# Kernel tuning notes

Hardware: AMD Instinct MI355X
Metric: run time of the kernel (lower is better)

Reference implementation:

```python
import jax, jax.numpy as jnp
import numpy as np

TEMP = 0.1          # temp1 == base_temperature -> scale factor temp/base = 1
N_VIEW = 100        # max_views


def _select_indices(hard, easy):
    """Deterministic analogue of _hard_anchor_sampling's per-(image,class) pick.
    hard, easy: [M, HW] bool. Returns [M, N_VIEW] pixel indices (hard first,
    then easy, in pixel-index order; torch uses randperm but the contrastive
    loss is invariant to which/ordering of in-set samples)."""
    half = N_VIEW // 2
    nh = hard.sum(-1)
    ne = easy.sum(-1)
    both = (nh >= half) & (ne >= half)
    hk = jnp.where(both, half, jnp.where(nh >= half, N_VIEW - ne, nh))  # num_hard_keep
    ek = N_VIEW - hk                                                     # num_easy_keep
    hrank = jnp.cumsum(hard.astype(jnp.int32), -1) - 1
    erank = jnp.cumsum(easy.astype(jnp.int32), -1) - 1
    sel = (hard & (hrank < hk[:, None])) | (easy & (erank < ek[:, None]))
    # stable argsort puts selected pixels first, preserving index order
    order = jnp.argsort(jnp.where(sel, 0, 1), axis=-1)
    return order[:, :N_VIEW]


def _contrastive(feats_, labels_):
    """feats_: [A, V, D], labels_: [A] float. Supervised contrastive loss."""
    A, V, D = feats_.shape
    N = A * V
    # torch.cat(torch.unbind(feats_, 1), 0) -> view-major ordering
    cf = feats_.transpose(1, 0, 2).reshape(N, D)
    lab = jnp.tile(labels_, V)                           # mask.repeat(V, V)
    mask = (lab[:, None] == lab[None, :]).astype(cf.dtype)
    logits = (cf @ cf.T) / TEMP                          # [N, N]
    logits = logits - jax.lax.stop_gradient(logits.max(axis=1, keepdims=True))
    neg_mask = 1.0 - mask                                # before removing diagonal
    pos_mask = mask * (1.0 - jnp.eye(N, dtype=cf.dtype)) # logits_mask zeroes diag
    exp_l = jnp.exp(logits)
    neg_sum = (exp_l * neg_mask).sum(axis=1, keepdims=True)
    log_prob = logits - jnp.log(exp_l + neg_sum)
    mean_log_prob_pos = (pos_mask * log_prob).sum(axis=1) / pos_mask.sum(axis=1)
    return -(TEMP / TEMP) * mean_log_prob_pos.mean()


def _forward(feats, predict, labels):
    B, D, H, W = feats.shape
    C = predict.shape[1]
    HW = H * W
    # F.normalize(feats, p=2, dim=1)
    norm = jnp.sqrt((feats * feats).sum(axis=1, keepdims=True))
    feats = feats / jnp.maximum(norm, 1e-12)
    # bilinear upsample of logits to (H, W), softmax, conf/argmax
    logits_up = jax.image.resize(predict, (B, C, H, W), method='linear')
    probs = jax.nn.softmax(logits_up, axis=1)
    pred = jnp.argmax(probs, axis=1)                     # [B, H, W] (conf unused by loss)
    # nearest resize of labels to (H, W) is identity here (same size)
    pred_f = pred.reshape(B, HW)
    lab_f = labels.reshape(B, HW)
    feats_f = feats.transpose(0, 2, 3, 1).reshape(B, HW, D)
    cls = jnp.arange(C)
    hard = (pred_f[:, None, :] == cls[None, :, None]) & (lab_f[:, None, :] != cls[None, :, None])
    easy = (pred_f[:, None, :] == cls[None, :, None]) & (lab_f[:, None, :] == cls[None, :, None])
    idx = _select_indices(hard.reshape(B * C, HW), easy.reshape(B * C, HW))  # [B*C, N_VIEW]
    b_idx = jnp.repeat(jnp.arange(B), C)
    X_ = feats_f[b_idx[:, None], idx]                    # [B*C, N_VIEW, D]
    y_ = jnp.tile(cls, B).astype(feats.dtype)            # [B*C]
    return _contrastive(X_, y_)


def setup_inputs() -> dict:
    key = jax.random.key(0)
    k1, k2, k3 = jax.random.split(key, 3)
    feats = jax.random.normal(k1, (4, 256, 128, 128), dtype=jnp.float32)
    predict = jax.random.normal(k2, (4, 21, 64, 64), dtype=jnp.float32)
    labels = jax.random.randint(k3, (4, 128, 128), 0, 21, dtype=jnp.int32)
    return {"feats": feats, "predict": predict, "labels": labels}


def reference(feats, predict, labels):
    return _forward(feats, predict, labels)
```

## Files before the change

kernel.cpp:

```cpp
#include <hip/hip_runtime.h>
#include <math.h>

#define HW 16384
#define WID 128
#define BB 4
#define CC 21
#define DD 256
#define NA 84
#define NV 100
#define NN 8400
#define NPOS 400
#define NPAD 8448
#define NTILE 66
#define NTRI 2211
#define NPOSBLK (16 * CC)

typedef __bf16 bf16;
typedef bf16 v8bf __attribute__((ext_vector_type(8)));
typedef float v4f __attribute__((ext_vector_type(4)));

#define AS1(p) ((const __attribute__((address_space(1))) void*)(p))
#define AS3(p) ((__attribute__((address_space(3))) void*)(p))

__global__ void pred_kernel(const float* __restrict__ predict, int* __restrict__ pred) {
  int t = blockIdx.x * blockDim.x + threadIdx.x;
  int b = t / HW;
  int p = t % HW;
  int y = p / WID, x = p % WID;
  float yin = y * 0.5f - 0.25f;
  float xin = x * 0.5f - 0.25f;
  int y0 = (int)floorf(yin), x0 = (int)floorf(xin);
  float fy = yin - (float)y0, fx = xin - (float)x0;
  int y0c = max(y0, 0), y1c = min(y0 + 1, 63);
  int x0c = max(x0, 0), x1c = min(x0 + 1, 63);
  float w00 = (1.f - fy) * (1.f - fx), w01 = (1.f - fy) * fx;
  float w10 = fy * (1.f - fx),        w11 = fy * fx;
  const float* pb = predict + (size_t)b * CC * 4096;
  float best = -1e30f; int bc = 0;
  for (int c = 0; c < CC; ++c) {
    const float* pc = pb + c * 4096;
    float v = w00 * pc[y0c * 64 + x0c] + w01 * pc[y0c * 64 + x1c]
            + w10 * pc[y1c * 64 + x0c] + w11 * pc[y1c * 64 + x1c];
    if (v > best) { best = v; bc = c; }
  }
  pred[t] = bc;
}

__global__ __launch_bounds__(256) void select_kernel(const int* __restrict__ pred,
                                                     const int* __restrict__ labels,
                                                     int* __restrict__ idx) {
  int pair = blockIdx.x;
  int b = pair / CC, c = pair % CC;
  int tid = threadIdx.x;
  const int4* pb = (const int4*)(pred + b * HW) + tid * 16;
  const int4* lb = (const int4*)(labels + b * HW) + tid * 16;

  unsigned long long hm = 0ull, em = 0ull;
  #pragma unroll
  for (int g = 0; g < 16; ++g) {
    int4 p4 = pb[g];
    int4 l4 = lb[g];
    unsigned long long h =
        ((unsigned long long)((p4.x == c) & (l4.x != c)))      |
        ((unsigned long long)((p4.y == c) & (l4.y != c)) << 1) |
        ((unsigned long long)((p4.z == c) & (l4.z != c)) << 2) |
        ((unsigned long long)((p4.w == c) & (l4.w != c)) << 3);
    unsigned long long e =
        ((unsigned long long)((p4.x == c) & (l4.x == c)))      |
        ((unsigned long long)((p4.y == c) & (l4.y == c)) << 1) |
        ((unsigned long long)((p4.z == c) & (l4.z == c)) << 2) |
        ((unsigned long long)((p4.w == c) & (l4.w == c)) << 3);
    hm |= h << (g * 4);
    em |= e << (g * 4);
  }
  int nh_t = __popcll(hm), ne_t = __popcll(em);

  __shared__ int sh[256], se[256], ss[256];
  sh[tid] = nh_t; se[tid] = ne_t;
  __syncthreads();
  for (int off = 1; off < 256; off <<= 1) {
    int vh = (tid >= off) ? sh[tid - off] : 0;
    int ve = (tid >= off) ? se[tid - off] : 0;
    __syncthreads();
    sh[tid] += vh; se[tid] += ve;
    __syncthreads();
  }
  int h_excl = sh[tid] - nh_t, e_excl = se[tid] - ne_t;
  int nh = sh[255], ne = se[255];

  const int half = NV / 2;
  int hk;
  if (nh >= half && ne >= half) hk = half;
  else if (nh >= half)          hk = NV - ne;
  else                          hk = nh;
  int ek = NV - hk;

  int takeh = min(max(hk - h_excl, 0), nh_t);
  int takee = min(max(ek - e_excl, 0), ne_t);
  int sel_t = takeh + takee;
  ss[tid] = sel_t;
  __syncthreads();
  for (int off = 1; off < 256; off <<= 1) {
    int vs = (tid >= off) ? ss[tid - off] : 0;
    __syncthreads();
    ss[tid] += vs;
    __syncthreads();
  }
  int s_excl = ss[tid] - sel_t;
  int total_sel = ss[255];
  int F = NV - total_sel;
  int u_excl = tid * 64 - s_excl;

  int* out = idx + pair * NV;
  int sc = 0, uc = 0, hc = 0, ec = 0;
  for (int l = 0; l < 64; ++l) {
    int p = tid * 64 + l;
    int hard = (int)((hm >> l) & 1ull);
    int easy = (int)((em >> l) & 1ull);
    bool sel = (hard && hc < takeh) || (easy && ec < takee);
    hc += hard; ec += easy;
    if (sel) {
      if (s_excl + sc < NV) out[s_excl + sc] = p;
      sc++;
    } else {
      if (u_excl + uc < F) out[total_sel + u_excl + uc] = p;
      uc++;
    }
  }
}

__global__ __launch_bounds__(256) void gather_kernel(const float* __restrict__ feats,
                                                     const int* __restrict__ idx,
                                                     bf16* __restrict__ cf) {
  int g = blockIdx.x;
  int d = threadIdx.x;
  if (g == 2100) {
    v8bf z = {};
    for (int e = d; e < (NPAD - NN) * DD / 8; e += 256)
      *(v8bf*)(cf + (size_t)NN * DD + e * 8) = z;
    return;
  }
  int a = g % NA;
  int v0 = (g / NA) * 4;
  int b = a / CC;

  int p[4];
  #pragma unroll
  for (int k = 0; k < 4; ++k) p[k] = idx[a * NV + v0 + k];
  const float* base = feats + (size_t)(b * DD + d) * HW;
  float val[4], ssk[4];
  #pragma unroll
  for (int k = 0; k < 4; ++k) { val[k] = base[p[k]]; ssk[k] = val[k] * val[k]; }

  #pragma unroll
  for (int k = 0; k < 4; ++k) {
    float s = ssk[k];
    s += __shfl_xor(s, 1);  s += __shfl_xor(s, 2);  s += __shfl_xor(s, 4);
    s += __shfl_xor(s, 8);  s += __shfl_xor(s, 16); s += __shfl_xor(s, 32);
    ssk[k] = s;
  }
  __shared__ float red[4][4];
  if ((d & 63) == 0) {
    #pragma unroll
    for (int k = 0; k < 4; ++k) red[d >> 6][k] = ssk[k];
  }
  __syncthreads();
  #pragma unroll
  for (int k = 0; k < 4; ++k) {
    float tot = red[0][k] + red[1][k] + red[2][k] + red[3][k];
    float inv = 1.0f / fmaxf(sqrtf(tot), 1e-12f);
    int n = (v0 + k) * NA + a;
    cf[(size_t)n * DD + d] = (bf16)(val[k] * inv);
  }
}

__global__ __launch_bounds__(256) void gemm_kernel(const bf16* __restrict__ cf,
                                                   float* __restrict__ row_part,
                                                   float* __restrict__ s_pos) {
  __shared__ __align__(16) bf16 smem[2 * 128 * 64];
  bf16* sA = smem;
  bf16* sB = smem + 128 * 64;
  int blk = blockIdx.x;
  bool pos = blk >= NTRI;
  int i0, j0, c = 0, I = 0, J = 0;
  bool diag = false;
  if (!pos) {
    I = (int)((sqrtf(8.0f * blk + 1.0f) - 1.0f) * 0.5f);
    while ((I + 1) * (I + 2) / 2 <= blk) ++I;
    while (I * (I + 1) / 2 > blk) --I;
    J = blk - I * (I + 1) / 2;
    i0 = I * 128;
    j0 = J * 128;
    diag = (I == J);
  } else {
    int pb = blk - NTRI;
    c = pb / 16;
    int bx = pb % 16;
    i0 = (bx >> 2) * 128;
    j0 = (bx & 3) * 128;
  }
  int tid = threadIdx.x;
  int wave = tid >> 6, lane = tid & 63;
  int wi = wave >> 1, wj = wave & 1;
  int m = lane & 15, q = lane >> 4;

  v4f acc[4][4] = {};

  int lrow = lane >> 3;
  int cxor = (lane & 7) ^ lrow;

  for (int k0 = 0; k0 < DD; k0 += 64) {
    #pragma unroll
    for (int it = 0; it < 4; ++it) {
      int row = wave * 32 + it * 8;
      int ri = i0 + row + lrow, rj = j0 + row + lrow;
      int gi, gj;
      if (!pos) { gi = ri; gj = rj; }
      else {
        gi = (ri < NPOS) ? ((ri >> 2) * NA + (ri & 3) * CC + c) : NN;
        gj = (rj < NPOS) ? ((rj >> 2) * NA + (rj & 3) * CC + c) : NN;
      }
      __builtin_amdgcn_global_load_lds(AS1(cf + (size_t)gi * DD + k0 + cxor * 8),
                                       AS3(sA + row * 64), 16, 0, 0);
      __builtin_amdgcn_global_load_lds(AS1(cf + (size_t)gj * DD + k0 + cxor * 8),
                                       AS3(sB + row * 64), 16, 0, 0);
    }
    __syncthreads();
    #pragma unroll
    for (int kk = 0; kk < 2; ++kk) {
      v8bf af[4], bfr[4];
      #pragma unroll
      for (int tt = 0; tt < 4; ++tt) {
        int r = wi * 64 + tt * 16 + m;
        af[tt] = *(const v8bf*)(sA + r * 64 + (((kk * 4 + q) ^ (m & 7)) * 8));
      }
      #pragma unroll
      for (int tt = 0; tt < 4; ++tt) {
        int r = wj * 64 + tt * 16 + m;
        bfr[tt] = *(const v8bf*)(sB + r * 64 + (((kk * 4 + q) ^ (m & 7)) * 8));
      }
      #pragma unroll
      for (int ti = 0; ti < 4; ++ti)
        #pragma unroll
        for (int tj = 0; tj < 4; ++tj)
          acc[ti][tj] = __builtin_amdgcn_mfma_f32_16x16x32_bf16(af[ti], bfr[tj], acc[ti][tj], 0, 0, 0);
    }
    __syncthreads();
  }

  if (!pos) {
    int iw0 = i0 + wi * 64;
    int jw0 = j0 + wj * 64;
    float rowp[16];
    float colp[4] = {0.f, 0.f, 0.f, 0.f};
    #pragma unroll
    for (int tt = 0; tt < 16; ++tt) rowp[tt] = 0.f;

    #pragma unroll
    for (int ti = 0; ti < 4; ++ti) {
      #pragma unroll
      for (int r = 0; r < 4; ++r) {
        int i = iw0 + ti * 16 + q * 4 + r;
        bool iok = (i < NN);
        #pragma unroll
        for (int tj = 0; tj < 4; ++tj) {
          int j = jw0 + tj * 16 + m;
          float e = __expf(acc[ti][tj][r] * 10.0f - 10.0f);
          if (j < NN) rowp[ti * 4 + r] += e;
          if (!diag && iok) colp[tj] += e;
        }
      }
    }

    float* redR = (float*)smem;
    float* redC = (float*)smem + 128 * 33;
    #pragma unroll
    for (int ti = 0; ti < 4; ++ti)
      #pragma unroll
      for (int r = 0; r < 4; ++r) {
        int rg = wi * 64 + ti * 16 + q * 4 + r;
        redR[rg * 33 + wj * 16 + m] = rowp[ti * 4 + r];
      }
    if (!diag) {
      #pragma unroll
      for (int tj = 0; tj < 4; ++tj) {
        int cg = wj * 64 + tj * 16 + m;
        redC[cg * 9 + wi * 4 + q] = colp[tj];
      }
    }
    __syncthreads();
    if (tid < 128) {
      float s = 0.f;
      #pragma unroll
      for (int t = 0; t < 32; ++t) s += redR[tid * 33 + t];
      row_part[(size_t)J * NPAD + i0 + tid] = s;
      if (!diag) {
        float s2 = 0.f;
        #pragma unroll
        for (int t = 0; t < 8; ++t) s2 += redC[tid * 9 + t];
        row_part[(size_t)I * NPAD + j0 + tid] = s2;
      }
    }
  } else {
    #pragma unroll
    for (int ti = 0; ti < 4; ++ti) {
      #pragma unroll
      for (int r = 0; r < 4; ++r) {
        int ri = i0 + wi * 64 + ti * 16 + q * 4 + r;
        if (ri >= NPOS) continue;
        int gi = (ri >> 2) * NA + (ri & 3) * CC + c;
        #pragma unroll
        for (int tj = 0; tj < 4; ++tj) {
          int rj = j0 + wj * 64 + tj * 16 + m;
          if (rj < NPOS)
            s_pos[(size_t)gi * NPOS + rj] = acc[ti][tj][r] * 10.0f - 10.0f;
        }
      }
    }
  }
}

__global__ __launch_bounds__(256) void loss_kernel(const float* __restrict__ s_pos,
                                                   const float* __restrict__ row_part,
                                                   double* __restrict__ partials) {
  int tid = threadIdx.x;
  int wave = tid >> 6, lane = tid & 63;
  int i = blockIdx.x * 4 + wave;
  const float* row = s_pos + (size_t)i * NPOS;

  float nsum = 0.f;
  for (int jb = lane; jb < NTILE; jb += 64)
    nsum += row_part[(size_t)jb * NPAD + i];

  float sp[7], ev[7];
  float psum = 0.f;
  #pragma unroll
  for (int t = 0; t < 7; ++t) {
    int k = lane + t * 64;
    if (k < NPOS) {
      sp[t] = row[k];
      ev[t] = __expf(sp[t]);
      psum += ev[t];
    } else { sp[t] = 0.f; ev[t] = 0.f; }
  }
  float comb = nsum - psum;
  for (int o = 32; o; o >>= 1) comb += __shfl_xor(comb, o);
  float ns = comb;

  int self = (i / NA) * 4 + ((i % NA) / CC);
  float tsum = 0.f;
  #pragma unroll
  for (int t = 0; t < 7; ++t) {
    int k = lane + t * 64;
    if (k < NPOS && k != self)
      tsum += sp[t] - __logf(ev[t] + ns);
  }
  for (int o = 32; o; o >>= 1) tsum += __shfl_xor(tsum, o);

  __shared__ float r2[4];
  if (lane == 0) r2[wave] = tsum;
  __syncthreads();
  if (tid == 0) partials[blockIdx.x] = (double)(r2[0] + r2[1] + r2[2] + r2[3]);
}

__global__ void final_kernel(const double* __restrict__ partials, float* __restrict__ out) {
  int lane = threadIdx.x;
  double s = 0.0;
  for (int t = lane; t < 2100; t += 64) s += partials[t];
  for (int o = 32; o; o >>= 1) s += __shfl_down(s, o);
  if (lane == 0) out[0] = (float)(-s / 399.0 / 8400.0);
}

extern "C" void kernel_launch(void* const* d_in, const int* in_sizes, int n_in,
                              void* d_out, int out_size, void* d_ws, size_t ws_size,
                              hipStream_t stream) {
  const float* feats   = (const float*)d_in[0];
  const float* predict = (const float*)d_in[1];
  const int*   labels  = (const int*)d_in[2];
  float* out = (float*)d_out;
  char* ws = (char*)d_ws;

  int*    pred     = (int*)(ws + 0);
  int*    idx      = (int*)(ws + 262144);
  float*  row_part = (float*)(ws + 295744);
  double* partials = (double*)(ws + 2526016);
  bf16*   cf       = (bf16*)(ws + 2542816);
  float*  s_pos    = (float*)(ws + 6868192);

  pred_kernel<<<256, 256, 0, stream>>>(predict, pred);
  select_kernel<<<NA, 256, 0, stream>>>(pred, labels, idx);
  gather_kernel<<<2101, 256, 0, stream>>>(feats, idx, cf);
  gemm_kernel<<<NTRI + NPOSBLK, 256, 0, stream>>>(cf, row_part, s_pos);
  loss_kernel<<<2100, 256, 0, stream>>>(s_pos, row_part, partials);
  final_kernel<<<1, 64, 0, stream>>>(partials, out);
}
```

Baseline: 185.4 us.

## Stream feats in coalesced pixel chunks via inverse index map instead of scattered gather

The index list is replaced by an inverse map from pixel to output row. The gather kernel now streams all of feats in coalesced 32-pixel chunks through shared memory, normalizes each pixel and writes only the mapped pixels. Unselected filler samples go through an atomic-appended fill list handled by dedicated blocks. This swaps strided scalar reads for full, coalesced reads of the feature tensor, and adds extra bandwidth plus an atomic counter.

```diff
diff --git a/kernel.cpp b/kernel.cpp
--- a/kernel.cpp
+++ b/kernel.cpp
@@ -14,16 +14,23 @@
 #define NTILE 66
 #define NTRI 2211
 #define NPOSBLK (16 * CC)
+#define PXC 32
+#define NCHUNK (BB * HW / PXC)
+#define NFILLB 84
 
 typedef __bf16 bf16;
 typedef bf16 v8bf __attribute__((ext_vector_type(8)));
+typedef bf16 v4bf __attribute__((ext_vector_type(4)));
 typedef float v4f __attribute__((ext_vector_type(4)));
 
 #define AS1(p) ((const __attribute__((address_space(1))) void*)(p))
 #define AS3(p) ((__attribute__((address_space(3))) void*)(p))
 
-__global__ void pred_kernel(const float* __restrict__ predict, int* __restrict__ pred) {
+__global__ void pred_kernel(const float* __restrict__ predict, int* __restrict__ pred,
+                            int* __restrict__ map, int* __restrict__ fill_cnt) {
   int t = blockIdx.x * blockDim.x + threadIdx.x;
+  if (t == 0) *fill_cnt = 0;
+  map[t] = -1;
   int b = t / HW;
   int p = t % HW;
   int y = p / WID, x = p % WID;
@@ -48,7 +55,9 @@
 
 __global__ __launch_bounds__(256) void select_kernel(const int* __restrict__ pred,
                                                      const int* __restrict__ labels,
-                                                     int* __restrict__ idx) {
+                                                     int* __restrict__ map,
+                                                     int2* __restrict__ fill_list,
+                                                     int* __restrict__ fill_cnt) {
   int pair = blockIdx.x;
   int b = pair / CC, c = pair % CC;
   int tid = threadIdx.x;
@@ -111,7 +120,6 @@
   int F = NV - total_sel;
   int u_excl = tid * 64 - s_excl;
 
-  int* out = idx + pair * NV;
   int sc = 0, uc = 0, hc = 0, ec = 0;
   for (int l = 0; l < 64; ++l) {
     int p = tid * 64 + l;
@@ -120,57 +128,99 @@
     bool sel = (hard && hc < takeh) || (easy && ec < takee);
     hc += hard; ec += easy;
     if (sel) {
-      if (s_excl + sc < NV) out[s_excl + sc] = p;
+      int v = s_excl + sc;
+      if (v < NV) map[b * HW + p] = v * NA + pair;
       sc++;
     } else {
-      if (u_excl + uc < F) out[total_sel + u_excl + uc] = p;
+      int v = total_sel + u_excl + uc;
+      if (u_excl + uc < F) {
+        int slot = atomicAdd(fill_cnt, 1);
+        fill_list[slot] = make_int2(v * NA + pair, p);
+      }
       uc++;
     }
   }
 }
 
 __global__ __launch_bounds__(256) void gather_kernel(const float* __restrict__ feats,
-                                                     const int* __restrict__ idx,
+                                                     const int* __restrict__ map,
+                                                     const int2* __restrict__ fill_list,
+                                                     const int* __restrict__ fill_cnt,
                                                      bf16* __restrict__ cf) {
+  __shared__ float tile[PXC * 257];
+  __shared__ float ssp[8][PXC];
+  __shared__ float inv_s[PXC];
+  __shared__ int sn[PXC], sx[PXC], scnt;
+  __shared__ float fred[4];
   int g = blockIdx.x;
-  int d = threadIdx.x;
-  if (g == 2100) {
+  int t = threadIdx.x;
+
+  if (g == NCHUNK) {
     v8bf z = {};
-    for (int e = d; e < (NPAD - NN) * DD / 8; e += 256)
+    for (int e = t; e < (NPAD - NN) * DD / 8; e += 256)
       *(v8bf*)(cf + (size_t)NN * DD + e * 8) = z;
     return;
   }
-  int a = g % NA;
-  int v0 = (g / NA) * 4;
-  int b = a / CC;
-
-  int p[4];
-  #pragma unroll
-  for (int k = 0; k < 4; ++k) p[k] = idx[a * NV + v0 + k];
-  const float* base = feats + (size_t)(b * DD + d) * HW;
-  float val[4], ssk[4];
-  #pragma unroll
-  for (int k = 0; k < 4; ++k) { val[k] = base[p[k]]; ssk[k] = val[k] * val[k]; }
-
-  #pragma unroll
-  for (int k = 0; k < 4; ++k) {
-    float s = ssk[k];
-    s += __shfl_xor(s, 1);  s += __shfl_xor(s, 2);  s += __shfl_xor(s, 4);
-    s += __shfl_xor(s, 8);  s += __shfl_xor(s, 16); s += __shfl_xor(s, 32);
-    ssk[k] = s;
-  }
-  __shared__ float red[4][4];
-  if ((d & 63) == 0) {
-    #pragma unroll
-    for (int k = 0; k < 4; ++k) red[d >> 6][k] = ssk[k];
-  }
+  if (g > NCHUNK) {
+    int cnt = *fill_cnt;
+    int d = t;
+    for (int e = g - NCHUNK - 1; e < cnt; e += NFILLB) {
+      int2 fe = fill_list[e];
+      int n = fe.x, p = fe.y;
+      int b = (n % NA) / CC;
+      float val = feats[((size_t)(b * DD + d)) * HW + p];
+      float ss = val * val;
+      for (int o = 32; o; o >>= 1) ss += __shfl_down(ss, o);
+      if ((d & 63) == 0) fred[d >> 6] = ss;
+      __syncthreads();
+      float tot = fred[0] + fred[1] + fred[2] + fred[3];
+      float inv = 1.0f / fmaxf(sqrtf(tot), 1e-12f);
+      cf[(size_t)n * DD + d] = (bf16)(val * inv);
+      __syncthreads();
+    }
+    return;
+  }
+
+  int b = g >> 9;
+  int p0 = (g & 511) * PXC;
+  int px = t & 31, dg = t >> 5;
+
+  const float* base = feats + ((size_t)b * DD + dg * 32) * HW + p0 + px;
+  float ss = 0.f;
+  #pragma unroll 8
+  for (int k = 0; k < 32; ++k) {
+    float v = base[(size_t)k * HW];
+    tile[px * 257 + dg * 32 + k] = v;
+    ss += v * v;
+  }
+  ssp[dg][px] = ss;
   __syncthreads();
-  #pragma unroll
-  for (int k = 0; k < 4; ++k) {
-    float tot = red[0][k] + red[1][k] + red[2][k] + red[3][k];
-    float inv = 1.0f / fmaxf(sqrtf(tot), 1e-12f);
-    int n = (v0 + k) * NA + a;
-    cf[(size_t)n * DD + d] = (bf16)(val[k] * inv);
+  if (t == 0) {
+    int cnum = 0;
+    for (int x = 0; x < PXC; ++x) {
+      int n = map[b * HW + p0 + x];
+      if (n >= 0) { sn[cnum] = n; sx[cnum] = x; ++cnum; }
+    }
+    scnt = cnum;
+  }
+  if (t < PXC) {
+    float tot = 0.f;
+    #pragma unroll
+    for (int j = 0; j < 8; ++j) tot += ssp[j][t];
+    inv_s[t] = 1.0f / fmaxf(sqrtf(tot), 1e-12f);
+  }
+  __syncthreads();
+
+  int wv = t >> 6, ln = t & 63;
+  for (int s = wv; s < scnt; s += 4) {
+    int n = sn[s], x = sx[s];
+    float inv = inv_s[x];
+    int d0 = ln * 4;
+    v4bf o;
+    #pragma unroll
+    for (int j = 0; j < 4; ++j)
+      o[j] = (bf16)(tile[x * 257 + d0 + j] * inv);
+    *(v4bf*)(cf + (size_t)n * DD + d0) = o;
   }
 }
 
@@ -380,16 +430,18 @@
   float* out = (float*)d_out;
   char* ws = (char*)d_ws;
 
-  int*    pred     = (int*)(ws + 0);
-  int*    idx      = (int*)(ws + 262144);
-  float*  row_part = (float*)(ws + 295744);
-  double* partials = (double*)(ws + 2526016);
-  bf16*   cf       = (bf16*)(ws + 2542816);
-  float*  s_pos    = (float*)(ws + 6868192);
-
-  pred_kernel<<<256, 256, 0, stream>>>(predict, pred);
-  select_kernel<<<NA, 256, 0, stream>>>(pred, labels, idx);
-  gather_kernel<<<2101, 256, 0, stream>>>(feats, idx, cf);
+  int*    pred      = (int*)(ws + 0);
+  int*    map       = (int*)(ws + 262144);
+  int*    fill_cnt  = (int*)(ws + 524288);
+  int2*   fill_list = (int2*)(ws + 524304);
+  float*  row_part  = (float*)(ws + 591504);
+  double* partials  = (double*)(ws + 2821776);
+  bf16*   cf        = (bf16*)(ws + 2838576);
+  float*  s_pos     = (float*)(ws + 7163952);
+
+  pred_kernel<<<256, 256, 0, stream>>>(predict, pred, map, fill_cnt);
+  select_kernel<<<NA, 256, 0, stream>>>(pred, labels, map, fill_list, fill_cnt);
+  gather_kernel<<<NCHUNK + 1 + NFILLB, 256, 0, stream>>>(feats, map, fill_list, fill_cnt, cf);
   gemm_kernel<<<NTRI + NPOSBLK, 256, 0, stream>>>(cf, row_part, s_pos);
   loss_kernel<<<2100, 256, 0, stream>>>(s_pos, row_part, partials);
   final_kernel<<<1, 64, 0, stream>>>(partials, out);
```

After: 176.8 us. 1.05x faster.
